# Optimization experiments

Measured on AMD Instinct MI355X. Metric: run time of the kernel, lower is better.

Reference implementation:

```python
import jax, jax.numpy as jnp
import numpy as np

N, R, E, H, D_MAX = 1024, 8192, 1024, 4, 48
DH = E // H
P_EDGE = 16.0 / R  # average in-degree ~16


def setup_inputs() -> dict:
    key = jax.random.key(0)
    ks = jax.random.split(key, 6)
    s = 0.02
    return {
        "target": jax.random.normal(ks[0], (N, E), jnp.float32),
        "source": jax.random.normal(ks[1], (R, E), jnp.float32),
        "adj": (jax.random.uniform(ks[2], (N, R)) < P_EDGE).astype(jnp.float32),
        "W_trans": jax.random.normal(ks[3], (E, E), jnp.float32) * s,
        "b_trans": jnp.zeros((E,), jnp.float32),
        "in_proj_w": jax.random.normal(ks[4], (3 * E, E), jnp.float32) * s,
        "in_proj_b": jnp.zeros((3 * E,), jnp.float32),
        "out_w": jax.random.normal(ks[5], (E, E), jnp.float32) * s,
        "out_b": jnp.zeros((E,), jnp.float32),
        "unit_id": 0,
    }


def reference(target, source, adj, W_trans, b_trans, in_proj_w, in_proj_b, out_w, out_b, unit_id):
    # source = relu(trans_fc(source))
    src = jax.nn.relu(source @ W_trans.T + b_trans)  # [R, E]

    # build padded neighbor index lists (torch loops per node; here vectorized)
    deg = adj.sum(axis=1).astype(jnp.int32)                # [N]
    order = jnp.argsort(-adj, axis=1)[:, :D_MAX]           # stable: 1-columns first, ascending col idx
    valid = jnp.arange(D_MAX)[None, :] < deg[:, None]      # [N, D] True = real neighbor
    neigh = jnp.where(valid, order, 0)                     # pad with index 0 (masked, like torch)
    kv_in = src[neigh]                                     # [N, D, E] gathered neighbor feats

    # nn.MultiheadAttention: q=target (len-1 query), k=v=padded neighbors
    Wq, Wk, Wv = jnp.split(in_proj_w, 3, axis=0)
    bq, bk, bv = jnp.split(in_proj_b, 3)
    q = (target @ Wq.T + bq).reshape(-1, H, DH)            # [N, H, dh]
    k = (kv_in @ Wk.T + bk).reshape(-1, D_MAX, H, DH)      # [N, D, H, dh]
    v = (kv_in @ Wv.T + bv).reshape(-1, D_MAX, H, DH)

    scores = jnp.einsum('nhd,nkhd->nhk', q, k) / np.float32(np.sqrt(DH))  # [N, H, D]
    # key_padding_mask: padded slots -> -inf; give zero-degree nodes one dummy
    # unmasked slot so softmax stays finite (their output is zeroed below)
    safe_valid = valid.at[:, 0].set(valid[:, 0] | (deg == 0))
    scores = jnp.where(safe_valid[:, None, :], scores, -jnp.inf)
    attn = jax.nn.softmax(scores, axis=-1)
    out = jnp.einsum('nhk,nkhd->nhd', attn, v).reshape(-1, E)
    out = out @ out_w.T + out_b

    # scatter back: inactive (degree-0) nodes stay zero, like att_res_padded
    return jnp.where((deg > 0)[:, None], out, jnp.zeros((), out.dtype))
```

## Files before the change

### kernel.cpp

```cpp
#include <hip/hip_runtime.h>

#define N_NODES 1024
#define R_SRC   8192
#define E_DIM   1024
#define H_HEADS 4
#define DH_DIM  256
#define D_MAXN  48

typedef __attribute__((ext_vector_type(8))) short short8;
typedef __attribute__((ext_vector_type(4))) float f32x4;

__device__ __forceinline__ unsigned short f2bf(float f) {
    unsigned u = __float_as_uint(f);
    unsigned r = u + 0x7fffu + ((u >> 16) & 1u);
    return (unsigned short)(r >> 16);
}
__device__ __forceinline__ float bf2f(unsigned short b) {
    return __uint_as_float(((unsigned)b) << 16);
}
__device__ __forceinline__ void gload16(const void* g, void* l) {
    __builtin_amdgcn_global_load_lds(
        (const __attribute__((address_space(1))) unsigned int*)g,
        (__attribute__((address_space(3))) unsigned int*)l,
        16, 0, 0);
}
template<int N> __device__ __forceinline__ void vwait() {
    if constexpr (N == 6)       asm volatile("s_waitcnt vmcnt(6)" ::: "memory");
    else if constexpr (N == 8)  asm volatile("s_waitcnt vmcnt(8)" ::: "memory");
    else                        asm volatile("s_waitcnt vmcnt(0)" ::: "memory");
}

struct GD {
    const unsigned short* A;
    const unsigned short* B;
    const float* bias;
    void* C;
    int N, K, nbx, relu, outbf;
    const int* rowmask;
};

template<int BM, int BN>
__global__ __launch_bounds__(512) void gemm_t(GD d0, GD d1, int split)
{
    constexpr int AI = BM / 64;
    constexpr int BI = BN / 64;
    constexpr int VN = AI + BI;
    constexpr int FM = BM / 32;
    constexpr int FN = BN / 64;

    __shared__ __align__(16) unsigned short lds[2][(BM + BN) * 64];

    int bid = blockIdx.x;
    const int nwg = gridDim.x;
    bid = (bid & 7) * (nwg >> 3) + (bid >> 3);

    GD d; int q;
    if (bid < split) { d = d0; q = bid; }
    else             { d = d1; q = bid - split; }
    const int m0 = (q / d.nbx) * BM;
    const int n0 = (q % d.nbx) * BN;
    const int K  = d.K;

    const int t = threadIdx.x;
    const int w = t >> 6, l = t & 63;
    const int wm = w >> 2, wn = w & 3;

    const int trow = t >> 3, tkc = t & 7;
    const int tswz = tkc ^ (trow & 7);
    const unsigned short* gA[AI];
    const unsigned short* gB[BI];
#pragma unroll
    for (int i = 0; i < AI; ++i)
        gA[i] = d.A + (size_t)(m0 + i * 64 + trow) * K + tswz * 8;
#pragma unroll
    for (int i = 0; i < BI; ++i)
        gB[i] = d.B + (size_t)(n0 + i * 64 + trow) * K + tswz * 8;

    f32x4 acc[FM][FN] = {};

    auto STAGE = [&](int c, int kt) {
        const int ko = kt * 64;
#pragma unroll
        for (int i = 0; i < AI; ++i)
            gload16(gA[i] + ko, &lds[c][(i * 512 + t) * 8]);
#pragma unroll
        for (int i = 0; i < BI; ++i)
            gload16(gB[i] + ko, &lds[c][BM * 64 + (i * 512 + t) * 8]);
    };

    const int nt = K / 64;
    STAGE(0, 0);
    STAGE(1, 1);
    vwait<VN>();
    __builtin_amdgcn_s_barrier();

    const int lr = l & 15, hi = l >> 4;
    const int rsw = l & 7;
    const int cs0 = ((0 + hi) ^ rsw) * 8;
    const int cs1 = ((4 + hi) ^ rsw) * 8;
    const int abase = (wm * (BM / 2) + lr) * 64;
    const int bbase = BM * 64 + (wn * 64 + lr) * 64;

    for (int kt = 0; kt < nt; ++kt) {
        const int cur = kt & 1;
        const unsigned short* Ls = &lds[cur][0];

        short8 bv[FN][2];
#pragma unroll
        for (int fj = 0; fj < FN; ++fj) {
            bv[fj][0] = *(const short8*)&Ls[bbase + fj * 1024 + cs0];
            bv[fj][1] = *(const short8*)&Ls[bbase + fj * 1024 + cs1];
        }
#pragma unroll
        for (int g = 0; g < FM; g += 4) {
            short8 av[4][2];
#pragma unroll
            for (int fi = 0; fi < 4; ++fi) {
                av[fi][0] = *(const short8*)&Ls[abase + (g + fi) * 1024 + cs0];
                av[fi][1] = *(const short8*)&Ls[abase + (g + fi) * 1024 + cs1];
            }
            __builtin_amdgcn_s_setprio(1);
#pragma unroll
            for (int ks = 0; ks < 2; ++ks)
#pragma unroll
                for (int fi = 0; fi < 4; ++fi)
#pragma unroll
                    for (int fj = 0; fj < FN; ++fj)
                        acc[g + fi][fj] = __builtin_amdgcn_mfma_f32_16x16x32_bf16(
                            av[fi][ks], bv[fj][ks], acc[g + fi][fj], 0, 0, 0);
            __builtin_amdgcn_s_setprio(0);
        }

        asm volatile("" ::: "memory");
        __builtin_amdgcn_s_barrier();
        if (kt + 2 < nt) {
            STAGE(cur, kt + 2);
            vwait<VN>();
        } else {
            vwait<0>();
        }
        __builtin_amdgcn_s_barrier();
    }

#pragma unroll
    for (int fj = 0; fj < FN; ++fj) {
        const int c = n0 + wn * 64 + fj * 16 + lr;
        const float bvs = d.bias[c];
#pragma unroll
        for (int fi = 0; fi < FM; ++fi) {
            const int rb = m0 + wm * (BM / 2) + fi * 16 + hi * 4;
#pragma unroll
            for (int qq = 0; qq < 4; ++qq) {
                const int r = rb + qq;
                float x = acc[fi][fj][qq] + bvs;
                if (d.relu) x = fmaxf(x, 0.0f);
                if (d.rowmask && d.rowmask[r] == 0) x = 0.0f;
                if (d.outbf) ((unsigned short*)d.C)[(size_t)r * d.N + c] = f2bf(x);
                else         ((float*)d.C)[(size_t)r * d.N + c] = x;
            }
        }
    }
}

struct GS {
    const unsigned short* A;
    const unsigned short* B;
    const float* bias;
    void* C;
    int lda, ldb, ldc, K, relu, outbf;
    long long azs, bzs, czs;
    int bias_zs;
    const int* rowmask;
};

__global__ __launch_bounds__(256) void gemm_s(GS g)
{
    const int z = blockIdx.z;
    const unsigned short* A = g.A + (size_t)((long long)z * g.azs);
    const unsigned short* B = g.B + (size_t)((long long)z * g.bzs);
    const float* bias = g.bias ? g.bias + (size_t)z * g.bias_zs : nullptr;

    __shared__ __align__(16) unsigned short S[128 * 32];

    const int t = threadIdx.x;
    const int m0 = blockIdx.y * 64;
    const int n0 = blockIdx.x * 64;
    const int w = t >> 6, l = t & 63;
    const int wrow = (w >> 1) * 32;
    const int wcol = (w & 1) * 32;
    const int lr = l & 15;
    const int kg = (l >> 4) * 8;

    f32x4 acc[2][2] = {};

    const unsigned short* gp[2];
    unsigned short* lp[2];
    {
        const int c0 = t;
        gp[0] = A + (size_t)(m0 + (c0 >> 2)) * g.lda + (c0 & 3) * 8;
        lp[0] = &S[c0 * 8];
        const int c1 = t;
        gp[1] = B + (size_t)(n0 + (c1 >> 2)) * g.ldb + (c1 & 3) * 8;
        lp[1] = &S[2048 + c1 * 8];
    }

    for (int k0 = 0; k0 < g.K; k0 += 32) {
        gload16(gp[0] + k0, lp[0]);
        gload16(gp[1] + k0, lp[1]);
        __syncthreads();

        short8 af[2], bw[2];
#pragma unroll
        for (int i = 0; i < 2; ++i)
            af[i] = *(const short8*)&S[(wrow + i * 16 + lr) * 32 + kg];
#pragma unroll
        for (int j = 0; j < 2; ++j)
            bw[j] = *(const short8*)&S[2048 + (wcol + j * 16 + lr) * 32 + kg];
#pragma unroll
        for (int i = 0; i < 2; ++i)
#pragma unroll
            for (int j = 0; j < 2; ++j)
                acc[i][j] = __builtin_amdgcn_mfma_f32_16x16x32_bf16(
                    af[i], bw[j], acc[i][j], 0, 0, 0);
        __syncthreads();
    }

#pragma unroll
    for (int j = 0; j < 2; ++j) {
        const int c = n0 + wcol + j * 16 + lr;
        const float bv = bias ? bias[c] : 0.0f;
#pragma unroll
        for (int i = 0; i < 2; ++i) {
            const int rbase = m0 + wrow + i * 16 + (l >> 4) * 4;
#pragma unroll
            for (int qq = 0; qq < 4; ++qq) {
                const int r = rbase + qq;
                float x = acc[i][j][qq] + bv;
                if (g.relu) x = fmaxf(x, 0.0f);
                if (g.rowmask && g.rowmask[r] == 0) x = 0.0f;
                if (g.outbf)
                    ((unsigned short*)g.C)[(size_t)((long long)z * g.czs) + (size_t)r * g.ldc + c] = f2bf(x);
                else
                    ((float*)g.C)[(size_t)((long long)z * g.czs) + (size_t)r * g.ldc + c] = x;
            }
        }
    }
}

struct ConvArgs {
    const float* s[5];
    unsigned short* d[5];
    unsigned off[6];
};

__global__ __launch_bounds__(256) void pre_kernel(
    const float* __restrict__ adj, int* __restrict__ neigh, int* __restrict__ deg,
    ConvArgs a, const float* __restrict__ inw_f, unsigned short* __restrict__ WkT,
    int nconv)
{
    const int t = threadIdx.x;

    if (blockIdx.x >= (unsigned)(N_NODES + nconv)) {
        __shared__ float tile[64][65];
        const int tb = blockIdx.x - N_NODES - nconv;
        const int h = tb >> 6, rem = tb & 63;
        const int e0 = (rem >> 2) * 64, d0 = (rem & 3) * 64;
        const int r = t >> 2, c4 = (t & 3) * 16;
        const float* tsrc = inw_f + (size_t)(E_DIM + h * 256 + d0 + r) * E_DIM + e0 + c4;
#pragma unroll
        for (int jj = 0; jj < 4; ++jj) {
            float4 v = ((const float4*)tsrc)[jj];
            tile[r][c4 + jj * 4 + 0] = v.x;
            tile[r][c4 + jj * 4 + 1] = v.y;
            tile[r][c4 + jj * 4 + 2] = v.z;
            tile[r][c4 + jj * 4 + 3] = v.w;
        }
        __syncthreads();
        const int er = t >> 2, dc = (t & 3) * 16;
        unsigned short* wout = WkT + ((size_t)h * E_DIM + e0 + er) * 256 + d0 + dc;
#pragma unroll
        for (int jj = 0; jj < 4; ++jj) {
            ushort4 o;
            o.x = f2bf(tile[dc + jj * 4 + 0][er]);
            o.y = f2bf(tile[dc + jj * 4 + 1][er]);
            o.z = f2bf(tile[dc + jj * 4 + 2][er]);
            o.w = f2bf(tile[dc + jj * 4 + 3][er]);
            ((ushort4*)wout)[jj] = o;
        }
        return;
    }

    if (blockIdx.x >= (unsigned)N_NODES) {
        unsigned i = (blockIdx.x - N_NODES) * 256 + t;
        if (i >= a.off[5]) return;
        int seg = 0;
#pragma unroll
        for (int s = 1; s < 5; ++s) seg += (i >= a.off[s]);
        unsigned j = i - a.off[seg];
        float4 v = ((const float4*)a.s[seg])[j];
        ushort4 o;
        o.x = f2bf(v.x); o.y = f2bf(v.y); o.z = f2bf(v.z); o.w = f2bf(v.w);
        ((ushort4*)a.d[seg])[j] = o;
        return;
    }

    const int n    = blockIdx.x;
    const int w    = t >> 6;
    const int lane = t & 63;
    const float* row = adj + (size_t)n * R_SRC;

    __shared__ int s_cnt[4];
    __shared__ int s_idx[4][D_MAXN];

    const int seg0 = w * (R_SRC / 4);
    const unsigned long long lower = (1ULL << lane) - 1ULL;
    int total = 0;

    for (int base = seg0; base < seg0 + R_SRC / 4; base += 256) {
        const float v0 = row[base + lane];
        const float v1 = row[base + 64 + lane];
        const float v2 = row[base + 128 + lane];
        const float v3 = row[base + 192 + lane];
        const unsigned long long m0 = __ballot(v0 != 0.0f);
        const unsigned long long m1 = __ballot(v1 != 0.0f);
        const unsigned long long m2 = __ballot(v2 != 0.0f);
        const unsigned long long m3 = __ballot(v3 != 0.0f);
        int p;
        p = total + __popcll(m0 & lower);
        if (v0 != 0.0f && p < D_MAXN) s_idx[w][p] = base + lane;
        total += __popcll(m0);
        p = total + __popcll(m1 & lower);
        if (v1 != 0.0f && p < D_MAXN) s_idx[w][p] = base + 64 + lane;
        total += __popcll(m1);
        p = total + __popcll(m2 & lower);
        if (v2 != 0.0f && p < D_MAXN) s_idx[w][p] = base + 128 + lane;
        total += __popcll(m2);
        p = total + __popcll(m3 & lower);
        if (v3 != 0.0f && p < D_MAXN) s_idx[w][p] = base + 192 + lane;
        total += __popcll(m3);
    }
    if (lane == 0) s_cnt[w] = total;
    __syncthreads();

    int start = 0;
#pragma unroll
    for (int i = 0; i < 4; ++i) if (i < w) start += s_cnt[i];
    const int degree = s_cnt[0] + s_cnt[1] + s_cnt[2] + s_cnt[3];
    const int nstore = total < D_MAXN ? total : D_MAXN;
    if (lane < nstore) {
        const int gpos = start + lane;
        if (gpos < D_MAXN) neigh[n * D_MAXN + gpos] = s_idx[w][lane];
    }
    if (t == 0) deg[n] = degree;
}

__global__ __launch_bounds__(256) void gather_ctx(
    const float* __restrict__ Ahat, const unsigned short* __restrict__ srcrel,
    const int* __restrict__ neigh, const int* __restrict__ deg,
    unsigned short* __restrict__ ctx)
{
    const int n = blockIdx.x;
    const int t = threadIdx.x;
    const int h = t >> 6;
    const int lane = t & 63;

    unsigned short* crow = ctx + ((size_t)n * H_HEADS + h) * E_DIM + lane * 16;
    const int degree = deg[n];
    if (degree == 0) {
        ushort4 z4 = {0, 0, 0, 0};
#pragma unroll
        for (int j = 0; j < 4; ++j) ((ushort4*)crow)[j] = z4;
        return;
    }
    const int dv = degree < D_MAXN ? degree : D_MAXN;

    __shared__ int s_neigh[D_MAXN];
    if (t < dv) s_neigh[t] = neigh[n * D_MAXN + t];
    __syncthreads();

    float a[16];
    {
        const float4* ap = (const float4*)(Ahat + (size_t)n * (H_HEADS * E_DIM) + h * E_DIM + lane * 16);
#pragma unroll
        for (int j = 0; j < 4; ++j) {
            float4 v = ap[j];
            a[j * 4 + 0] = v.x; a[j * 4 + 1] = v.y; a[j * 4 + 2] = v.z; a[j * 4 + 3] = v.w;
        }
    }

    float m = -3.4e38f, sum = 0.0f;
    float cacc[16];
#pragma unroll
    for (int i = 0; i < 16; ++i) cacc[i] = 0.0f;

    for (int d = 0; d < dv; ++d) {
        const int r = s_neigh[d];
        const ushort4* rp = (const ushort4*)(srcrel + (size_t)r * E_DIM + lane * 16);
        float e[16];
#pragma unroll
        for (int j = 0; j < 4; ++j) {
            ushort4 v = rp[j];
            e[j * 4 + 0] = bf2f(v.x); e[j * 4 + 1] = bf2f(v.y);
            e[j * 4 + 2] = bf2f(v.z); e[j * 4 + 3] = bf2f(v.w);
        }
        float s = 0.0f;
#pragma unroll
        for (int i = 0; i < 16; ++i) s = fmaf(a[i], e[i], s);
#pragma unroll
        for (int off = 32; off > 0; off >>= 1) s += __shfl_xor(s, off);
        s *= 0.0625f;

        if (s > m) {
            const float f = __expf(m - s);
            sum *= f;
#pragma unroll
            for (int i = 0; i < 16; ++i) cacc[i] *= f;
            m = s;
        }
        const float wgt = __expf(s - m);
        sum += wgt;
#pragma unroll
        for (int i = 0; i < 16; ++i) cacc[i] = fmaf(wgt, e[i], cacc[i]);
    }

    const float inv = 1.0f / sum;
#pragma unroll
    for (int j = 0; j < 4; ++j) {
        ushort4 o;
        o.x = f2bf(cacc[j * 4 + 0] * inv);
        o.y = f2bf(cacc[j * 4 + 1] * inv);
        o.z = f2bf(cacc[j * 4 + 2] * inv);
        o.w = f2bf(cacc[j * 4 + 3] * inv);
        ((ushort4*)crow)[j] = o;
    }
}

extern "C" void kernel_launch(void* const* d_in, const int* in_sizes, int n_in,
                              void* d_out, int out_size, void* d_ws, size_t ws_size,
                              hipStream_t stream)
{
    const float* target  = (const float*)d_in[0];
    const float* source  = (const float*)d_in[1];
    const float* adj     = (const float*)d_in[2];
    const float* W_trans = (const float*)d_in[3];
    const float* b_trans = (const float*)d_in[4];
    const float* in_w    = (const float*)d_in[5];
    const float* in_b    = (const float*)d_in[6];
    const float* out_w   = (const float*)d_in[7];
    const float* out_b   = (const float*)d_in[8];
    float* out = (float*)d_out;

    char* ws = (char*)d_ws;
    unsigned short* src_bf    = (unsigned short*)ws; ws += (size_t)R_SRC * E_DIM * 2;
    unsigned short* wt_bf     = (unsigned short*)ws; ws += (size_t)E_DIM * E_DIM * 2;
    unsigned short* inw_bf    = (unsigned short*)ws; ws += (size_t)3 * E_DIM * E_DIM * 2;
    unsigned short* outw_bf   = (unsigned short*)ws; ws += (size_t)E_DIM * E_DIM * 2;
    unsigned short* tgt_bf    = (unsigned short*)ws; ws += (size_t)N_NODES * E_DIM * 2;
    unsigned short* srcrel_bf = (unsigned short*)ws; ws += (size_t)R_SRC * E_DIM * 2;
    unsigned short* WkT_bf    = (unsigned short*)ws; ws += (size_t)H_HEADS * E_DIM * DH_DIM * 2;
    unsigned short* Q_bf      = (unsigned short*)ws; ws += (size_t)N_NODES * E_DIM * 2;
    float*          Ahat      = (float*)ws;         ws += (size_t)N_NODES * H_HEADS * E_DIM * 4;
    unsigned short* ctx_bf    = (unsigned short*)ws; ws += (size_t)N_NODES * H_HEADS * E_DIM * 2;
    unsigned short* attn_bf   = (unsigned short*)ws; ws += (size_t)N_NODES * E_DIM * 2;
    int*            neigh     = (int*)ws;            ws += (size_t)N_NODES * D_MAXN * 4;
    int*            deg       = (int*)ws;            ws += (size_t)N_NODES * 4;

    const size_t EE = (size_t)E_DIM * E_DIM;

    {
        ConvArgs a;
        const unsigned sz4[5] = {
            (unsigned)((size_t)R_SRC * E_DIM / 4),
            (unsigned)(EE / 4),
            (unsigned)(3 * EE / 4),
            (unsigned)(EE / 4),
            (unsigned)((size_t)N_NODES * E_DIM / 4)};
        a.s[0] = source;  a.d[0] = src_bf;
        a.s[1] = W_trans; a.d[1] = wt_bf;
        a.s[2] = in_w;    a.d[2] = inw_bf;
        a.s[3] = out_w;   a.d[3] = outw_bf;
        a.s[4] = target;  a.d[4] = tgt_bf;
        a.off[0] = 0;
        for (int i = 0; i < 5; ++i) a.off[i + 1] = a.off[i] + sz4[i];
        const int nconv = (int)((a.off[5] + 255) / 256);
        pre_kernel<<<N_NODES + nconv + 256, 256, 0, stream>>>(
            adj, neigh, deg, a, in_w, WkT_bf, nconv);
    }

    {
        GD ds;
        ds.A = src_bf; ds.B = wt_bf; ds.bias = b_trans; ds.C = srcrel_bf;
        ds.N = E_DIM; ds.K = E_DIM; ds.nbx = E_DIM / 256; ds.relu = 1; ds.outbf = 1;
        ds.rowmask = nullptr;
        const int sblocks = (R_SRC / 128) * (E_DIM / 256);
        gemm_t<128, 256><<<sblocks, 512, 0, stream>>>(ds, ds, sblocks);
    }

    {
        GS g;
        g.A = tgt_bf; g.B = inw_bf; g.bias = in_b; g.C = Q_bf;
        g.lda = E_DIM; g.ldb = E_DIM; g.ldc = E_DIM; g.K = E_DIM;
        g.relu = 0; g.outbf = 1; g.azs = 0; g.bzs = 0; g.czs = 0; g.bias_zs = 0;
        g.rowmask = nullptr;
        gemm_s<<<dim3(E_DIM / 64, N_NODES / 64, 1), 256, 0, stream>>>(g);
    }

    {
        GS g;
        g.A = Q_bf; g.B = WkT_bf; g.bias = nullptr; g.C = Ahat;
        g.lda = E_DIM; g.ldb = DH_DIM; g.ldc = H_HEADS * E_DIM; g.K = DH_DIM;
        g.relu = 0; g.outbf = 0;
        g.azs = DH_DIM;
        g.bzs = (long long)E_DIM * DH_DIM;
        g.czs = E_DIM;
        g.bias_zs = 0; g.rowmask = nullptr;
        gemm_s<<<dim3(E_DIM / 64, N_NODES / 64, H_HEADS), 256, 0, stream>>>(g);
    }

    gather_ctx<<<N_NODES, 256, 0, stream>>>(Ahat, srcrel_bf, neigh, deg, ctx_bf);

    {
        GS g;
        g.A = ctx_bf; g.B = inw_bf + 2 * EE; g.bias = in_b + 2 * E_DIM; g.C = attn_bf;
        g.lda = H_HEADS * E_DIM; g.ldb = E_DIM; g.ldc = E_DIM; g.K = E_DIM;
        g.relu = 0; g.outbf = 1;
        g.azs = E_DIM;
        g.bzs = (long long)DH_DIM * E_DIM;
        g.czs = DH_DIM;
        g.bias_zs = DH_DIM; g.rowmask = nullptr;
        gemm_s<<<dim3(DH_DIM / 64, N_NODES / 64, H_HEADS), 256, 0, stream>>>(g);
    }

    {
        GS g;
        g.A = attn_bf; g.B = outw_bf; g.bias = out_b; g.C = out;
        g.lda = E_DIM; g.ldb = E_DIM; g.ldc = E_DIM; g.K = E_DIM;
        g.relu = 0; g.outbf = 0; g.azs = 0; g.bzs = 0; g.czs = 0; g.bias_zs = 0;
        g.rowmask = deg;
        gemm_s<<<dim3(E_DIM / 64, N_NODES / 64, 1), 256, 0, stream>>>(g);
    }
}
```

Measured before the change: 128.0 us.

## Stage neighbor rows in LDS with double-buffered async loads in gather_ctx

The attention gather kernel used to have each of the four head-waves load the same neighbor row from global memory. It now loads each row once per block into LDS via global_load_lds, double-buffered so the next neighbor's row is prefetched while the current one is consumed. Per-lane element mapping changes to a strided lane+64k layout to avoid LDS bank conflicts. The cost is two block barriers per neighbor iteration and narrower, strided global accesses for the Ahat reads and ctx stores.

```diff
diff --git a/kernel.cpp b/kernel.cpp
--- a/kernel.cpp
+++ b/kernel.cpp
@@ -25,8 +25,9 @@
         16, 0, 0);
 }
 template<int N> __device__ __forceinline__ void vwait() {
-    if constexpr (N == 6)       asm volatile("s_waitcnt vmcnt(6)" ::: "memory");
-    else if constexpr (N == 8)  asm volatile("s_waitcnt vmcnt(8)" ::: "memory");
+    if constexpr (N == 8)       asm volatile("s_waitcnt vmcnt(8)" ::: "memory");
+    else if constexpr (N == 6)  asm volatile("s_waitcnt vmcnt(6)" ::: "memory");
+    else if constexpr (N == 1)  asm volatile("s_waitcnt vmcnt(1)" ::: "memory");
     else                        asm volatile("s_waitcnt vmcnt(0)" ::: "memory");
 }
 
@@ -364,48 +365,56 @@
     const int h = t >> 6;
     const int lane = t & 63;
 
-    unsigned short* crow = ctx + ((size_t)n * H_HEADS + h) * E_DIM + lane * 16;
+    unsigned short* crow = ctx + ((size_t)n * H_HEADS + h) * E_DIM;
     const int degree = deg[n];
     if (degree == 0) {
-        ushort4 z4 = {0, 0, 0, 0};
-#pragma unroll
-        for (int j = 0; j < 4; ++j) ((ushort4*)crow)[j] = z4;
+#pragma unroll
+        for (int k = 0; k < 16; ++k) crow[lane + 64 * k] = 0;
         return;
     }
     const int dv = degree < D_MAXN ? degree : D_MAXN;
 
     __shared__ int s_neigh[D_MAXN];
+    __shared__ __align__(16) unsigned short s_row[2][E_DIM];
+
     if (t < dv) s_neigh[t] = neigh[n * D_MAXN + t];
-    __syncthreads();
 
     float a[16];
     {
-        const float4* ap = (const float4*)(Ahat + (size_t)n * (H_HEADS * E_DIM) + h * E_DIM + lane * 16);
-#pragma unroll
-        for (int j = 0; j < 4; ++j) {
-            float4 v = ap[j];
-            a[j * 4 + 0] = v.x; a[j * 4 + 1] = v.y; a[j * 4 + 2] = v.z; a[j * 4 + 3] = v.w;
-        }
+        const float* ap = Ahat + ((size_t)n * H_HEADS + h) * E_DIM + lane;
+#pragma unroll
+        for (int k = 0; k < 16; ++k) a[k] = ap[64 * k];
     }
 
     float m = -3.4e38f, sum = 0.0f;
     float cacc[16];
 #pragma unroll
-    for (int i = 0; i < 16; ++i) cacc[i] = 0.0f;
+    for (int k = 0; k < 16; ++k) cacc[k] = 0.0f;
+
+    __syncthreads();
+
+    if (t < 128)
+        gload16(srcrel + (size_t)s_neigh[0] * E_DIM + t * 8, &s_row[0][t * 8]);
 
     for (int d = 0; d < dv; ++d) {
-        const int r = s_neigh[d];
-        const ushort4* rp = (const ushort4*)(srcrel + (size_t)r * E_DIM + lane * 16);
+        const int cur = d & 1;
+        if (d + 1 < dv) {
+            if (t < 128)
+                gload16(srcrel + (size_t)s_neigh[d + 1] * E_DIM + t * 8,
+                        &s_row[cur ^ 1][t * 8]);
+            vwait<1>();
+        } else {
+            vwait<0>();
+        }
+        __builtin_amdgcn_s_barrier();
+
         float e[16];
-#pragma unroll
-        for (int j = 0; j < 4; ++j) {
-            ushort4 v = rp[j];
-            e[j * 4 + 0] = bf2f(v.x); e[j * 4 + 1] = bf2f(v.y);
-            e[j * 4 + 2] = bf2f(v.z); e[j * 4 + 3] = bf2f(v.w);
-        }
         float s = 0.0f;
 #pragma unroll
-        for (int i = 0; i < 16; ++i) s = fmaf(a[i], e[i], s);
+        for (int k = 0; k < 16; ++k) {
+            e[k] = bf2f(s_row[cur][lane + 64 * k]);
+            s = fmaf(a[k], e[k], s);
+        }
 #pragma unroll
         for (int off = 32; off > 0; off >>= 1) s += __shfl_xor(s, off);
         s *= 0.0625f;
@@ -414,25 +423,22 @@
             const float f = __expf(m - s);
             sum *= f;
 #pragma unroll
-            for (int i = 0; i < 16; ++i) cacc[i] *= f;
+            for (int k = 0; k < 16; ++k) cacc[k] *= f;
             m = s;
         }
         const float wgt = __expf(s - m);
         sum += wgt;
 #pragma unroll
-        for (int i = 0; i < 16; ++i) cacc[i] = fmaf(wgt, e[i], cacc[i]);
+        for (int k = 0; k < 16; ++k) cacc[k] = fmaf(wgt, e[k], cacc[k]);
+
+        asm volatile("" ::: "memory");
+        __builtin_amdgcn_s_barrier();
     }
 
     const float inv = 1.0f / sum;
 #pragma unroll
-    for (int j = 0; j < 4; ++j) {
-        ushort4 o;
-        o.x = f2bf(cacc[j * 4 + 0] * inv);
-        o.y = f2bf(cacc[j * 4 + 1] * inv);
-        o.z = f2bf(cacc[j * 4 + 2] * inv);
-        o.w = f2bf(cacc[j * 4 + 3] * inv);
-        ((ushort4*)crow)[j] = o;
-    }
+    for (int k = 0; k < 16; ++k)
+        crow[lane + 64 * k] = f2bf(cacc[k] * inv);
 }
 
 extern "C" void kernel_launch(void* const* d_in, const int* in_sizes, int n_in,
```

Result: slower. 132.7 us (+3.7%).
